# Optimization experiments

Measured on AMD Instinct MI355X. Metric: run time of the kernel, lower is better.

Reference implementation:

```python
import jax, jax.numpy as jnp
import numpy as np

B, NA, E, H = 256, 128, 1024, 16
HD = E // H  # head_dim = 64
EPS = 1e-5


def _ln(x, w, b):
    m = x.mean(-1, keepdims=True)
    v = x.var(-1, keepdims=True)
    return (x - m) / jnp.sqrt(v + EPS) * w + b


def setup_inputs() -> dict:
    key = jax.random.key(0)
    k0, k1 = jax.random.split(key)
    return {
        "x": jax.random.normal(k0, (B, NA, E), jnp.float32),
        "ln1_w": jnp.ones((E,), jnp.float32),
        "ln1_b": jnp.zeros((E,), jnp.float32),
        # xavier_uniform-ish scale for (3E, E)
        "in_w": jax.random.normal(k1, (3 * E, E), jnp.float32) * (1.0 / np.sqrt(E)),
        "in_b": jnp.zeros((3 * E,), jnp.float32),
        "ln2_w": jnp.ones((E,), jnp.float32),
        "ln2_b": jnp.zeros((E,), jnp.float32),
    }


def reference(x, ln1_w, ln1_b, in_w, in_b, ln2_w, ln2_b):
    bsz, na, e = x.shape
    xn = _ln(x, ln1_w, ln1_b)  # x = ln1(x) in the original (residual uses this)
    qkv = xn @ in_w.T + in_b  # (bsz, na, 3E)
    q, k, v = jnp.split(qkv, 3, axis=-1)
    q = q * (float(HD) ** -0.5)
    # Faithful to torch's contiguous().view(na, bsz*H, HD).transpose(0, 1):
    # a raw row-major reshape of the (bsz, na, E) buffer.
    def _heads(t):
        return t.reshape(na, bsz * H, HD).swapaxes(0, 1)  # (bsz*H, na, HD)
    q, k, v = _heads(q), _heads(k), _heads(v)
    scores = jnp.einsum('bnd,bmd->bnm', q, k)  # (bsz*H, na, na)
    w = jax.nn.softmax(scores, axis=-1)
    attn = jnp.einsum('bnm,bmd->bnd', w, v)  # (bsz*H, na, HD)
    attn = attn.swapaxes(0, 1).reshape(bsz, na, e)
    out = _ln(xn + attn, ln2_w, ln2_b)
    # Faithful quirk: sum over dim=1 (query dim) of (bsz*H, na, na), / num_heads
    avg_w = w.sum(axis=1) / H  # (bsz*H, na)
    return out, avg_w
```

## Files before the change

kernel.cpp:

```cpp
#include <hip/hip_runtime.h>


typedef __attribute__((ext_vector_type(4))) float float4v;
typedef __attribute__((ext_vector_type(4))) int   int4v;
typedef __attribute__((ext_vector_type(8))) short short8v;
typedef __attribute__((ext_vector_type(4))) short short4v;

#define LN_EPS 1e-5f

#define GLL(g, l) __builtin_amdgcn_global_load_lds( \
    (const __attribute__((address_space(1))) unsigned int*)(g), \
    (__attribute__((address_space(3))) unsigned int*)(l), 16, 0, 0)

__device__ __forceinline__ unsigned short f2bf(float f) {
    unsigned int u = __float_as_uint(f);
    u += 0x7FFFu + ((u >> 16) & 1u);
    return (unsigned short)(u >> 16);
}
__device__ __forceinline__ float bf2f(unsigned short h) {
    return __uint_as_float(((unsigned int)h) << 16);
}

__global__ __launch_bounds__(256) void k0_w_to_bf16(const float* __restrict__ w,
                                                    unsigned short* __restrict__ wb) {
    int idx = blockIdx.x * 256 + threadIdx.x;
    const float4v* src = (const float4v*)w;
    float4v a = src[idx * 2];
    float4v b = src[idx * 2 + 1];
    short8v o;
    o[0] = (short)f2bf(a[0]); o[1] = (short)f2bf(a[1]);
    o[2] = (short)f2bf(a[2]); o[3] = (short)f2bf(a[3]);
    o[4] = (short)f2bf(b[0]); o[5] = (short)f2bf(b[1]);
    o[6] = (short)f2bf(b[2]); o[7] = (short)f2bf(b[3]);
    *((short8v*)wb + idx) = o;
}

__global__ __launch_bounds__(256) void k1_ln1(const float* __restrict__ x,
                                              const float* __restrict__ w1,
                                              const float* __restrict__ b1,
                                              unsigned short* __restrict__ xnb) {
    int lane = threadIdx.x & 63;
    int wave = threadIdx.x >> 6;
    int row  = blockIdx.x * 4 + wave;
    const float4v* xr = (const float4v*)(x + (size_t)row * 1024);
    float4v xv[4];
    float s = 0.f, s2 = 0.f;
    #pragma unroll
    for (int c = 0; c < 4; ++c) {
        xv[c] = xr[c * 64 + lane];
        #pragma unroll
        for (int e = 0; e < 4; ++e) { s += xv[c][e]; s2 += xv[c][e] * xv[c][e]; }
    }
    #pragma unroll
    for (int off = 32; off > 0; off >>= 1) {
        s  += __shfl_xor(s, off, 64);
        s2 += __shfl_xor(s2, off, 64);
    }
    float mean = s * (1.0f / 1024.0f);
    float var  = s2 * (1.0f / 1024.0f) - mean * mean;
    float rs   = rsqrtf(var + LN_EPS);
    #pragma unroll
    for (int c = 0; c < 4; ++c) {
        int idx = c * 64 + lane;
        float4v wv = ((const float4v*)w1)[idx];
        float4v bv = ((const float4v*)b1)[idx];
        short4v o;
        #pragma unroll
        for (int e = 0; e < 4; ++e)
            o[e] = (short)f2bf((xv[c][e] - mean) * rs * wv[e] + bv[e]);
        ((short4v*)(xnb + (size_t)row * 1024))[idx] = o;
    }
}

__global__ __launch_bounds__(512, 2) void k2_qkv_gemm(const unsigned short* __restrict__ A,
                                                      const unsigned short* __restrict__ W,
                                                      const float* __restrict__ bias,
                                                      unsigned short* __restrict__ Qb,
                                                      unsigned short* __restrict__ Kb,
                                                      unsigned short* __restrict__ Vb) {
    __shared__ unsigned short smem[65536];
    unsigned short* sA0 = smem;
    unsigned short* sA1 = smem + 16384;
    unsigned short* sB0 = smem + 32768;
    unsigned short* sB1 = smem + 49152;

    int bid = blockIdx.x;
    int wg  = (bid & 7) * 192 + (bid >> 3);
    int nT  = wg % 12;
    int mT  = wg / 12;
    int rowBase = mT * 256;
    int colBase = nT * 256;

    int tid  = threadIdx.x;
    int lane = tid & 63;
    int wave = tid >> 6;
    int wm = wave >> 2, wn = wave & 3;
    int q4 = lane >> 4, l15 = lane & 15;

    int lrow_s = tid >> 3;
    int srcCol = ((tid & 7) * 16) ^ ((lrow_s & 7) << 4);
    const char* aSrc = (const char*)A + ((size_t)(rowBase + lrow_s) << 11) + srcCol;
    const char* wSrc = (const char*)W + ((size_t)(colBase + lrow_s) << 11) + srcCol;
    int waveOff = wave * 1024;

    int xorv = (l15 & 7) << 4;
    int aRow = (wm * 128 + l15) * 128;
    int bRow = (wn * 64 + l15) * 128;
    int bc0 = (q4 * 16) ^ xorv;
    int bc1 = (64 + q4 * 16) ^ xorv;

    float bv[4];
    #pragma unroll
    for (int n = 0; n < 4; ++n) bv[n] = bias[colBase + wn * 64 + n * 16 + l15];

    float4v acc[8][4];
    #pragma unroll
    for (int t = 0; t < 8; ++t)
        #pragma unroll
        for (int n = 0; n < 4; ++n) acc[t][n] = (float4v){0.f, 0.f, 0.f, 0.f};

#define STAGE_HALF(lds, src, ktB_, h) do { \
    GLL((src) + (ktB_) + (2*(h))   * 131072, (char*)(lds) + (2*(h))   * 8192 + waveOff); \
    GLL((src) + (ktB_) + (2*(h)+1) * 131072, (char*)(lds) + (2*(h)+1) * 8192 + waveOff); \
} while (0)
#define LDB(SB) do { \
    const char* c_ = (const char*)(SB); \
    _Pragma("unroll") \
    for (int n = 0; n < 4; ++n) { \
        bf[n][0] = *(const short8v*)(c_ + bRow + n * 2048 + bc0); \
        bf[n][1] = *(const short8v*)(c_ + bRow + n * 2048 + bc1); \
    } \
} while (0)
#define LDA2(SA, T0_) do { \
    const char* c_ = (const char*)(SA); \
    af[0][0] = *(const short8v*)(c_ + aRow + (T0_)     * 2048 + bc0); \
    af[0][1] = *(const short8v*)(c_ + aRow + (T0_)     * 2048 + bc1); \
    af[1][0] = *(const short8v*)(c_ + aRow + (T0_ + 1) * 2048 + bc0); \
    af[1][1] = *(const short8v*)(c_ + aRow + (T0_ + 1) * 2048 + bc1); \
} while (0)
#define MFMA8(T0_) do { \
    __builtin_amdgcn_s_setprio(1); \
    _Pragma("unroll") \
    for (int n = 0; n < 4; ++n) { \
        acc[T0_][n]     = __builtin_amdgcn_mfma_f32_16x16x32_bf16(af[0][0], bf[n][0], acc[T0_][n], 0, 0, 0); \
        acc[T0_][n]     = __builtin_amdgcn_mfma_f32_16x16x32_bf16(af[0][1], bf[n][1], acc[T0_][n], 0, 0, 0); \
        acc[T0_ + 1][n] = __builtin_amdgcn_mfma_f32_16x16x32_bf16(af[1][0], bf[n][0], acc[T0_ + 1][n], 0, 0, 0); \
        acc[T0_ + 1][n] = __builtin_amdgcn_mfma_f32_16x16x32_bf16(af[1][1], bf[n][1], acc[T0_ + 1][n], 0, 0, 0); \
    } \
    __builtin_amdgcn_s_setprio(0); \
} while (0)
#define PH_SYNC do { __builtin_amdgcn_s_barrier(); asm volatile("s_waitcnt lgkmcnt(0)"); } while (0)
#define PH_END  __builtin_amdgcn_s_barrier()

    STAGE_HALF(sA0, aSrc, 0, 0);
    STAGE_HALF(sA0, aSrc, 0, 1);
    STAGE_HALF(sB0, wSrc, 0, 0);
    STAGE_HALF(sB0, wSrc, 0, 1);
    STAGE_HALF(sB1, wSrc, 128, 0);
    STAGE_HALF(sB1, wSrc, 128, 1);
    asm volatile("s_waitcnt vmcnt(4)");
    __builtin_amdgcn_s_barrier();

    short8v af[2][2], bf[4][2];

    #pragma unroll 1
    for (int i = 0; i < 8; ++i) {
        int ktB = i << 8;
        bool nl = (i < 7);
        LDB(sB0); LDA2(sA0, 0);
        STAGE_HALF(sA1, aSrc, ktB + 128, 0);
        PH_SYNC; MFMA8(0); PH_END;
        LDA2(sA0, 2);
        STAGE_HALF(sA1, aSrc, ktB + 128, 1);
        PH_SYNC; MFMA8(2); PH_END;
        LDA2(sA0, 4);
        if (nl) STAGE_HALF(sB0, wSrc, ktB + 256, 0);
        PH_SYNC; MFMA8(4); PH_END;
        LDA2(sA0, 6);
        if (nl) { STAGE_HALF(sB0, wSrc, ktB + 256, 1); asm volatile("s_waitcnt vmcnt(4)"); }
        else    { asm volatile("s_waitcnt vmcnt(0)"); }
        PH_SYNC; MFMA8(6); PH_END;
        LDB(sB1); LDA2(sA1, 0);
        if (nl) STAGE_HALF(sA0, aSrc, ktB + 256, 0);
        PH_SYNC; MFMA8(0); PH_END;
        LDA2(sA1, 2);
        if (nl) STAGE_HALF(sA0, aSrc, ktB + 256, 1);
        PH_SYNC; MFMA8(2); PH_END;
        LDA2(sA1, 4);
        if (nl) STAGE_HALF(sB1, wSrc, ktB + 384, 0);
        PH_SYNC; MFMA8(4); PH_END;
        LDA2(sA1, 6);
        if (nl) { STAGE_HALF(sB1, wSrc, ktB + 384, 1); asm volatile("s_waitcnt vmcnt(4)"); }
        PH_SYNC; MFMA8(6); PH_END;
    }
#undef STAGE_HALF
#undef LDB
#undef LDA2
#undef MFMA8
#undef PH_SYNC
#undef PH_END

    __syncthreads();
    float scale = (colBase < 1024) ? 0.125f : 1.0f;
    unsigned short* outb = (colBase < 1024) ? Qb : (colBase < 2048) ? Kb : Vb;
    int lcol = colBase & 1023;
    #pragma unroll
    for (int t = 0; t < 8; ++t)
        #pragma unroll
        for (int n = 0; n < 4; ++n)
            #pragma unroll
            for (int g = 0; g < 4; ++g) {
                int row  = wm * 128 + t * 16 + q4 * 4 + g;
                int colb = (wn * 64 + n * 16 + l15) * 2;
                *(unsigned short*)((char*)smem + row * 512 + (colb ^ ((row & 7) << 4))) =
                    f2bf((acc[t][n][g] + bv[n]) * scale);
            }
    __syncthreads();
    #pragma unroll
    for (int k = 0; k < 16; ++k) {
        int r = k * 16 + (tid >> 5);
        short8v v = *(const short8v*)((const char*)smem + r * 512 + (tid & 31) * 16);
        int colb = ((tid & 31) * 16) ^ ((r & 7) << 4);
        *(short8v*)((char*)(outb + (size_t)(rowBase + r) * 1024 + lcol) + colb) = v;
    }
}

__global__ __launch_bounds__(256) void k2b_vtrans(const unsigned short* __restrict__ Vb,
                                                  unsigned short* __restrict__ Vt) {
    int g  = blockIdx.x * 256 + threadIdx.x;
    int ib = g & 15;
    int db = (g >> 4) & 7;
    int j  = g >> 7;
    const unsigned short* src = Vb + (size_t)(ib * 8) * 262144 + (size_t)j * 64 + db * 8;
    short8v in[8];
    #pragma unroll
    for (int r = 0; r < 8; ++r)
        in[r] = *(const short8v*)(src + (size_t)r * 262144);
    unsigned short* dst = Vt + (size_t)j * 8192 + (db * 8) * 128 + ib * 8;
    #pragma unroll
    for (int c = 0; c < 8; ++c) {
        short8v o;
        #pragma unroll
        for (int r = 0; r < 8; ++r) o[r] = in[r][c];
        *(short8v*)(dst + c * 128) = o;
    }
}

#define P_S  136
__global__ __launch_bounds__(256) void k3_attn(const unsigned short* __restrict__ Qb,
                                               const unsigned short* __restrict__ Kb,
                                               const unsigned short* __restrict__ Vt,
                                               unsigned short* __restrict__ attnb,
                                               float* __restrict__ avgw) {
    __shared__ unsigned short region0[17408];
    __shared__ float wred[2][2][128];
    __shared__ float colsum[128];
    unsigned short* sQ = region0;
    unsigned short* sK = region0 + 8192;
    unsigned short* sP = region0;

    int j = blockIdx.x;
    int tid = threadIdx.x;
    int lane = tid & 63;
    int wave = tid >> 6;
    int wm = wave >> 1, wn = wave & 1;
    int q4 = lane >> 4, l15 = lane & 15;
    size_t base = (size_t)j * 64;

    if (tid < 128) colsum[tid] = 0.f;

    {
        const char* qg = (const char*)(Qb + base);
        const char* kg = (const char*)(Kb + base);
        int swz = ((lane & 7) ^ (lane >> 3)) << 4;
        #pragma unroll
        for (int blk = 0; blk < 4; ++blk) {
            int row0 = wave * 32 + blk * 8;
            size_t src = (size_t)(row0 + (lane >> 3)) * 524288 + swz;
            GLL(qg + src, (char*)sQ + row0 * 128);
            GLL(kg + src, (char*)sK + row0 * 128);
        }
    }
    __syncthreads();

    const char* vg = (const char*)(Vt + (size_t)j * 8192);
    short8v vf[4][2];
    #pragma unroll
    for (int ks = 0; ks < 4; ++ks)
        #pragma unroll
        for (int t = 0; t < 2; ++t)
            vf[ks][t] = *(const short8v*)(vg + (wn * 32 + t * 16 + l15) * 256 + ks * 64 + q4 * 16);

    float4v zero4 = {0.f, 0.f, 0.f, 0.f};
    float4v S[4][4];
    #pragma unroll
    for (int a = 0; a < 4; ++a)
        #pragma unroll
        for (int b = 0; b < 4; ++b) S[a][b] = zero4;
    #pragma unroll
    for (int ks = 0; ks < 2; ++ks) {
        short8v qf[4], kf[4];
        #pragma unroll
        for (int t = 0; t < 4; ++t) {
            int rq = (wm * 64 + t * 16 + l15) * 128;
            int rk = (wn * 64 + t * 16 + l15) * 128;
            int cb = (ks * 64 + q4 * 16) ^ ((l15 & 7) << 4);
            qf[t] = *(const short8v*)((const char*)sQ + rq + cb);
            kf[t] = *(const short8v*)((const char*)sK + rk + cb);
        }
        #pragma unroll
        for (int tm = 0; tm < 4; ++tm)
            #pragma unroll
            for (int tn = 0; tn < 4; ++tn)
                S[tm][tn] = __builtin_amdgcn_mfma_f32_16x16x32_bf16(qf[tm], kf[tn], S[tm][tn], 0, 0, 0);
    }

    float rmax[4][4];
    #pragma unroll
    for (int tm = 0; tm < 4; ++tm)
        #pragma unroll
        for (int g = 0; g < 4; ++g)
            rmax[tm][g] = fmaxf(fmaxf(S[tm][0][g], S[tm][1][g]), fmaxf(S[tm][2][g], S[tm][3][g]));
    #pragma unroll
    for (int off = 1; off <= 8; off <<= 1)
        #pragma unroll
        for (int tm = 0; tm < 4; ++tm)
            #pragma unroll
            for (int g = 0; g < 4; ++g)
                rmax[tm][g] = fmaxf(rmax[tm][g], __shfl_xor(rmax[tm][g], off, 64));
    if (l15 == 0) {
        #pragma unroll
        for (int tm = 0; tm < 4; ++tm)
            #pragma unroll
            for (int g = 0; g < 4; ++g)
                wred[0][wn][wm * 64 + tm * 16 + q4 * 4 + g] = rmax[tm][g];
    }
    __syncthreads();

    float rsum[4][4];
    #pragma unroll
    for (int tm = 0; tm < 4; ++tm)
        #pragma unroll
        for (int g = 0; g < 4; ++g) {
            int r = wm * 64 + tm * 16 + q4 * 4 + g;
            float rm = fmaxf(wred[0][0][r], wred[0][1][r]);
            float t0 = 0.f;
            #pragma unroll
            for (int tn = 0; tn < 4; ++tn) {
                float e = __expf(S[tm][tn][g] - rm);
                S[tm][tn][g] = e;
                t0 += e;
            }
            rsum[tm][g] = t0;
        }
    #pragma unroll
    for (int off = 1; off <= 8; off <<= 1)
        #pragma unroll
        for (int tm = 0; tm < 4; ++tm)
            #pragma unroll
            for (int g = 0; g < 4; ++g)
                rsum[tm][g] += __shfl_xor(rsum[tm][g], off, 64);
    if (l15 == 0) {
        #pragma unroll
        for (int tm = 0; tm < 4; ++tm)
            #pragma unroll
            for (int g = 0; g < 4; ++g)
                wred[1][wn][wm * 64 + tm * 16 + q4 * 4 + g] = rsum[tm][g];
    }
    __syncthreads();

    #pragma unroll
    for (int tm = 0; tm < 4; ++tm)
        #pragma unroll
        for (int g = 0; g < 4; ++g) {
            int r = wm * 64 + tm * 16 + q4 * 4 + g;
            float inv = 1.0f / (wred[1][0][r] + wred[1][1][r]);
            #pragma unroll
            for (int tn = 0; tn < 4; ++tn) S[tm][tn][g] *= inv;
        }

    float cs[4];
    #pragma unroll
    for (int tn = 0; tn < 4; ++tn) {
        float t0 = 0.f;
        #pragma unroll
        for (int tm = 0; tm < 4; ++tm)
            #pragma unroll
            for (int g = 0; g < 4; ++g) t0 += S[tm][tn][g];
        cs[tn] = t0;
    }
    #pragma unroll
    for (int off = 16; off <= 32; off <<= 1)
        #pragma unroll
        for (int tn = 0; tn < 4; ++tn) cs[tn] += __shfl_xor(cs[tn], off, 64);
    if (lane < 16) {
        #pragma unroll
        for (int tn = 0; tn < 4; ++tn)
            atomicAdd(&colsum[wn * 64 + tn * 16 + lane], cs[tn]);
    }
    __syncthreads();

    #pragma unroll
    for (int tm = 0; tm < 4; ++tm)
        #pragma unroll
        for (int tn = 0; tn < 4; ++tn)
            #pragma unroll
            for (int g = 0; g < 4; ++g)
                sP[(wm * 64 + tm * 16 + q4 * 4 + g) * P_S + wn * 64 + tn * 16 + l15] = f2bf(S[tm][tn][g]);
    __syncthreads();

    if (tid < 128) avgw[(size_t)j * 128 + tid] = colsum[tid] * (1.0f / 16.0f);

    float4v O[4][2];
    #pragma unroll
    for (int a = 0; a < 4; ++a) { O[a][0] = zero4; O[a][1] = zero4; }
    #pragma unroll
    for (int ks = 0; ks < 4; ++ks) {
        short8v pf[4];
        #pragma unroll
        for (int t = 0; t < 4; ++t)
            pf[t] = *(const short8v*)(sP + (wm * 64 + t * 16 + l15) * P_S + q4 * 8 + ks * 32);
        #pragma unroll
        for (int tm = 0; tm < 4; ++tm)
            #pragma unroll
            for (int tn = 0; tn < 2; ++tn)
                O[tm][tn] = __builtin_amdgcn_mfma_f32_16x16x32_bf16(pf[tm], vf[ks][tn], O[tm][tn], 0, 0, 0);
    }
    #pragma unroll
    for (int tm = 0; tm < 4; ++tm)
        #pragma unroll
        for (int tn = 0; tn < 2; ++tn)
            #pragma unroll
            for (int g = 0; g < 4; ++g) {
                int i = wm * 64 + tm * 16 + q4 * 4 + g;
                int d = wn * 32 + tn * 16 + l15;
                attnb[base + (size_t)i * 262144 + d] = f2bf(O[tm][tn][g]);
            }
}

__global__ __launch_bounds__(256) void k4_ln2(const float* __restrict__ x,
                                              const float* __restrict__ w1,
                                              const float* __restrict__ b1,
                                              const unsigned short* __restrict__ attnb,
                                              const float* __restrict__ w2,
                                              const float* __restrict__ b2,
                                              float* __restrict__ out) {
    int lane = threadIdx.x & 63;
    int wave = threadIdx.x >> 6;
    int row  = blockIdx.x * 4 + wave;
    const float4v* xr = (const float4v*)(x + (size_t)row * 1024);
    float4v xv[4];
    float s = 0.f, s2 = 0.f;
    #pragma unroll
    for (int c = 0; c < 4; ++c) {
        xv[c] = xr[c * 64 + lane];
        #pragma unroll
        for (int e = 0; e < 4; ++e) { s += xv[c][e]; s2 += xv[c][e] * xv[c][e]; }
    }
    #pragma unroll
    for (int off = 32; off > 0; off >>= 1) {
        s  += __shfl_xor(s, off, 64);
        s2 += __shfl_xor(s2, off, 64);
    }
    float mean = s * (1.0f / 1024.0f);
    float var  = s2 * (1.0f / 1024.0f) - mean * mean;
    float rs   = rsqrtf(var + LN_EPS);
    float4v r[4];
    s = 0.f; s2 = 0.f;
    #pragma unroll
    for (int c = 0; c < 4; ++c) {
        int idx = c * 64 + lane;
        float4v wv = ((const float4v*)w1)[idx];
        float4v bv = ((const float4v*)b1)[idx];
        short4v av = ((const short4v*)(attnb + (size_t)row * 1024))[idx];
        #pragma unroll
        for (int e = 0; e < 4; ++e) {
            r[c][e] = (xv[c][e] - mean) * rs * wv[e] + bv[e] + bf2f((unsigned short)av[e]);
            s += r[c][e]; s2 += r[c][e] * r[c][e];
        }
    }
    #pragma unroll
    for (int off = 32; off > 0; off >>= 1) {
        s  += __shfl_xor(s, off, 64);
        s2 += __shfl_xor(s2, off, 64);
    }
    float mean2 = s * (1.0f / 1024.0f);
    float var2  = s2 * (1.0f / 1024.0f) - mean2 * mean2;
    float rs2   = rsqrtf(var2 + LN_EPS);
    #pragma unroll
    for (int c = 0; c < 4; ++c) {
        int idx = c * 64 + lane;
        float4v w2v = ((const float4v*)w2)[idx];
        float4v b2v = ((const float4v*)b2)[idx];
        float4v o;
        #pragma unroll
        for (int e = 0; e < 4; ++e)
            o[e] = (r[c][e] - mean2) * rs2 * w2v[e] + b2v[e];
        ((float4v*)(out + (size_t)row * 1024))[idx] = o;
    }
}

extern "C" void kernel_launch(void* const* d_in, const int* in_sizes, int n_in,
                              void* d_out, int out_size, void* d_ws, size_t ws_size,
                              hipStream_t stream) {
    const float* x    = (const float*)d_in[0];
    const float* ln1w = (const float*)d_in[1];
    const float* ln1b = (const float*)d_in[2];
    const float* inw  = (const float*)d_in[3];
    const float* inb  = (const float*)d_in[4];
    const float* ln2w = (const float*)d_in[5];
    const float* ln2b = (const float*)d_in[6];
    float* out  = (float*)d_out;
    float* avgw = out + 33554432;

    char* ws = (char*)d_ws;
    unsigned short* xnb   = (unsigned short*)(ws);
    unsigned short* Vt    = (unsigned short*)(ws);
    unsigned short* Qb    = (unsigned short*)(ws + 67108864);
    unsigned short* Kb    = (unsigned short*)(ws + 134217728);
    unsigned short* Vb    = (unsigned short*)(ws + 201326592);
    unsigned short* attnb = (unsigned short*)(ws + 201326592);
    unsigned short* Wb    = (unsigned short*)(ws + 268435456);

    k0_w_to_bf16<<<1536, 256, 0, stream>>>(inw, Wb);
    k1_ln1<<<8192, 256, 0, stream>>>(x, ln1w, ln1b, xnb);
    k2_qkv_gemm<<<1536, 512, 0, stream>>>(xnb, Wb, inb, Qb, Kb, Vb);
    k2b_vtrans<<<2048, 256, 0, stream>>>(Vb, Vt);
    k3_attn<<<4096, 256, 0, stream>>>(Qb, Kb, Vt, attnb, avgw);
    k4_ln2<<<8192, 256, 0, stream>>>(x, ln1w, ln1b, attnb, ln2w, ln2b, out);
}
```

Before: 613.0 us.

## Restructure attention kernel: two heads per block, wave owns full score rows

The attention kernel now processes two heads per block, and each pair of waves splits one head by query rows, so every wave holds complete 128-wide score rows. It computes S transposed (K×Q) so that the row max and sum need only cross-lane shuffles, which removes the cross-wave LDS reductions and most of the block barriers. Each wave gets a private P buffer in LDS, writes bf16 values packed in pairs with v_cvt_pk_bf16, and double-buffers its V fragment loads across the PV k-steps. In exchange it uses more LDS per block (about 68KB), which may lower occupancy, and the score accumulators double per wave, which raises register pressure.

```diff
diff --git a/kernel.cpp b/kernel.cpp
--- a/kernel.cpp
+++ b/kernel.cpp
@@ -19,6 +19,11 @@
 }
 __device__ __forceinline__ float bf2f(unsigned short h) {
     return __uint_as_float(((unsigned int)h) << 16);
+}
+__device__ __forceinline__ unsigned int pk_bf16(float lo, float hi) {
+    unsigned int r;
+    asm("v_cvt_pk_bf16_f32 %0, %1, %2" : "=v"(r) : "v"(lo), "v"(hi));
+    return r;
 }
 
 __global__ __launch_bounds__(256) void k0_w_to_bf16(const float* __restrict__ w,
@@ -246,36 +251,35 @@
     }
 }
 
-#define P_S  136
 __global__ __launch_bounds__(256) void k3_attn(const unsigned short* __restrict__ Qb,
                                                const unsigned short* __restrict__ Kb,
                                                const unsigned short* __restrict__ Vt,
                                                unsigned short* __restrict__ attnb,
                                                float* __restrict__ avgw) {
-    __shared__ unsigned short region0[17408];
-    __shared__ float wred[2][2][128];
-    __shared__ float colsum[128];
-    unsigned short* sQ = region0;
-    unsigned short* sK = region0 + 8192;
-    unsigned short* sP = region0;
-
-    int j = blockIdx.x;
+    __shared__ unsigned short smem[34816];
+    __shared__ float csum[2][2][128];
+
     int tid = threadIdx.x;
     int lane = tid & 63;
     int wave = tid >> 6;
-    int wm = wave >> 1, wn = wave & 1;
+    int grp = wave >> 1, wm = wave & 1;
+    int j = blockIdx.x * 2 + grp;
     int q4 = lane >> 4, l15 = lane & 15;
-    size_t base = (size_t)j * 64;
-
-    if (tid < 128) colsum[tid] = 0.f;
+
+    unsigned short* sQ = smem + grp * 8192;
+    unsigned short* sK = smem + 16384 + grp * 8192;
+    char* sP = (char*)smem + wave * 17408;
+
+    csum[0][tid >> 7][tid & 127] = 0.f;
+    csum[1][tid >> 7][tid & 127] = 0.f;
 
     {
-        const char* qg = (const char*)(Qb + base);
-        const char* kg = (const char*)(Kb + base);
+        const char* qg = (const char*)(Qb + (size_t)j * 64);
+        const char* kg = (const char*)(Kb + (size_t)j * 64);
         int swz = ((lane & 7) ^ (lane >> 3)) << 4;
         #pragma unroll
-        for (int blk = 0; blk < 4; ++blk) {
-            int row0 = wave * 32 + blk * 8;
+        for (int blk = 0; blk < 8; ++blk) {
+            int row0 = wm * 64 + blk * 8;
             size_t src = (size_t)(row0 + (lane >> 3)) * 524288 + swz;
             GLL(qg + src, (char*)sQ + row0 * 128);
             GLL(kg + src, (char*)sK + row0 * 128);
@@ -283,159 +287,135 @@
     }
     __syncthreads();
 
-    const char* vg = (const char*)(Vt + (size_t)j * 8192);
-    short8v vf[4][2];
-    #pragma unroll
-    for (int ks = 0; ks < 4; ++ks)
-        #pragma unroll
-        for (int t = 0; t < 2; ++t)
-            vf[ks][t] = *(const short8v*)(vg + (wn * 32 + t * 16 + l15) * 256 + ks * 64 + q4 * 16);
-
-    float4v zero4 = {0.f, 0.f, 0.f, 0.f};
-    float4v S[4][4];
-    #pragma unroll
-    for (int a = 0; a < 4; ++a)
-        #pragma unroll
-        for (int b = 0; b < 4; ++b) S[a][b] = zero4;
+    float4v S[8][4];
+    #pragma unroll
+    for (int a = 0; a < 8; ++a)
+        #pragma unroll
+        for (int b = 0; b < 4; ++b) S[a][b] = (float4v){0.f, 0.f, 0.f, 0.f};
     #pragma unroll
     for (int ks = 0; ks < 2; ++ks) {
-        short8v qf[4], kf[4];
-        #pragma unroll
-        for (int t = 0; t < 4; ++t) {
-            int rq = (wm * 64 + t * 16 + l15) * 128;
-            int rk = (wn * 64 + t * 16 + l15) * 128;
-            int cb = (ks * 64 + q4 * 16) ^ ((l15 & 7) << 4);
-            qf[t] = *(const short8v*)((const char*)sQ + rq + cb);
-            kf[t] = *(const short8v*)((const char*)sK + rk + cb);
+        int cb = (ks * 64 + q4 * 16) ^ ((l15 & 7) << 4);
+        short8v qf[4];
+        #pragma unroll
+        for (int tm = 0; tm < 4; ++tm)
+            qf[tm] = *(const short8v*)((const char*)sQ + (wm * 64 + tm * 16 + l15) * 128 + cb);
+        #pragma unroll
+        for (int tn = 0; tn < 8; ++tn) {
+            short8v kf = *(const short8v*)((const char*)sK + (tn * 16 + l15) * 128 + cb);
+            #pragma unroll
+            for (int tm = 0; tm < 4; ++tm)
+                S[tn][tm] = __builtin_amdgcn_mfma_f32_16x16x32_bf16(kf, qf[tm], S[tn][tm], 0, 0, 0);
         }
-        #pragma unroll
-        for (int tm = 0; tm < 4; ++tm)
-            #pragma unroll
-            for (int tn = 0; tn < 4; ++tn)
-                S[tm][tn] = __builtin_amdgcn_mfma_f32_16x16x32_bf16(qf[tm], kf[tn], S[tm][tn], 0, 0, 0);
-    }
-
-    float rmax[4][4];
-    #pragma unroll
-    for (int tm = 0; tm < 4; ++tm)
-        #pragma unroll
-        for (int g = 0; g < 4; ++g)
-            rmax[tm][g] = fmaxf(fmaxf(S[tm][0][g], S[tm][1][g]), fmaxf(S[tm][2][g], S[tm][3][g]));
-    #pragma unroll
-    for (int off = 1; off <= 8; off <<= 1)
-        #pragma unroll
-        for (int tm = 0; tm < 4; ++tm)
-            #pragma unroll
-            for (int g = 0; g < 4; ++g)
-                rmax[tm][g] = fmaxf(rmax[tm][g], __shfl_xor(rmax[tm][g], off, 64));
-    if (l15 == 0) {
-        #pragma unroll
-        for (int tm = 0; tm < 4; ++tm)
-            #pragma unroll
-            for (int g = 0; g < 4; ++g)
-                wred[0][wn][wm * 64 + tm * 16 + q4 * 4 + g] = rmax[tm][g];
     }
     __syncthreads();
 
-    float rsum[4][4];
-    #pragma unroll
-    for (int tm = 0; tm < 4; ++tm)
-        #pragma unroll
-        for (int g = 0; g < 4; ++g) {
-            int r = wm * 64 + tm * 16 + q4 * 4 + g;
-            float rm = fmaxf(wred[0][0][r], wred[0][1][r]);
-            float t0 = 0.f;
-            #pragma unroll
-            for (int tn = 0; tn < 4; ++tn) {
-                float e = __expf(S[tm][tn][g] - rm);
-                S[tm][tn][g] = e;
+    const char* vg = (const char*)Vt + (size_t)j * 16384;
+    short8v vf0[4], vf1[4];
+    #pragma unroll
+    for (int t = 0; t < 4; ++t)
+        vf0[t] = *(const short8v*)(vg + (t * 16 + l15) * 256 + q4 * 16);
+
+    float rmax[4], inv[4];
+    #pragma unroll
+    for (int tm = 0; tm < 4; ++tm) {
+        float m0 = S[0][tm][0];
+        #pragma unroll
+        for (int tn = 0; tn < 8; ++tn)
+            #pragma unroll
+            for (int g = 0; g < 4; ++g) m0 = fmaxf(m0, S[tn][tm][g]);
+        m0 = fmaxf(m0, __shfl_xor(m0, 16, 64));
+        m0 = fmaxf(m0, __shfl_xor(m0, 32, 64));
+        rmax[tm] = m0;
+    }
+    #pragma unroll
+    for (int tm = 0; tm < 4; ++tm) {
+        float t0 = 0.f;
+        #pragma unroll
+        for (int tn = 0; tn < 8; ++tn)
+            #pragma unroll
+            for (int g = 0; g < 4; ++g) {
+                float e = __expf(S[tn][tm][g] - rmax[tm]);
+                S[tn][tm][g] = e;
                 t0 += e;
             }
-            rsum[tm][g] = t0;
+        t0 += __shfl_xor(t0, 16, 64);
+        t0 += __shfl_xor(t0, 32, 64);
+        inv[tm] = 1.0f / t0;
+    }
+    #pragma unroll
+    for (int tn = 0; tn < 8; ++tn)
+        #pragma unroll
+        for (int tm = 0; tm < 4; ++tm)
+            #pragma unroll
+            for (int g = 0; g < 4; ++g) S[tn][tm][g] *= inv[tm];
+
+    #pragma unroll
+    for (int tn = 0; tn < 8; ++tn) {
+        #pragma unroll
+        for (int g = 0; g < 4; ++g) {
+            float cs = S[tn][0][g] + S[tn][1][g] + S[tn][2][g] + S[tn][3][g];
+            cs += __shfl_xor(cs, 1, 64);
+            cs += __shfl_xor(cs, 2, 64);
+            cs += __shfl_xor(cs, 4, 64);
+            cs += __shfl_xor(cs, 8, 64);
+            if (l15 == 0) csum[wm][grp][tn * 16 + q4 * 4 + g] = cs;
         }
-    #pragma unroll
-    for (int off = 1; off <= 8; off <<= 1)
+    }
+
+    #pragma unroll
+    for (int tn = 0; tn < 8; ++tn)
         #pragma unroll
         for (int tm = 0; tm < 4; ++tm)
             #pragma unroll
-            for (int g = 0; g < 4; ++g)
-                rsum[tm][g] += __shfl_xor(rsum[tm][g], off, 64);
-    if (l15 == 0) {
+            for (int p = 0; p < 2; ++p) {
+                unsigned int pk = pk_bf16(S[tn][tm][2 * p], S[tn][tm][2 * p + 1]);
+                *(unsigned int*)(sP + (tm * 16 + l15) * 272 +
+                                 (tn * 16 + q4 * 4 + 2 * p) * 2) = pk;
+            }
+
+    float4v O[4][4];
+    #pragma unroll
+    for (int a = 0; a < 4; ++a)
+        #pragma unroll
+        for (int b = 0; b < 4; ++b) O[a][b] = (float4v){0.f, 0.f, 0.f, 0.f};
+    #pragma unroll
+    for (int ks = 0; ks < 4; ++ks) {
+        if (ks < 3) {
+            #pragma unroll
+            for (int t = 0; t < 4; ++t)
+                vf1[t] = *(const short8v*)(vg + (t * 16 + l15) * 256 + (ks + 1) * 64 + q4 * 16);
+        }
+        short8v pf[4];
         #pragma unroll
         for (int tm = 0; tm < 4; ++tm)
-            #pragma unroll
-            for (int g = 0; g < 4; ++g)
-                wred[1][wn][wm * 64 + tm * 16 + q4 * 4 + g] = rsum[tm][g];
-    }
+            pf[tm] = *(const short8v*)(sP + (tm * 16 + l15) * 272 + ks * 64 + q4 * 16);
+        #pragma unroll
+        for (int tm = 0; tm < 4; ++tm)
+            #pragma unroll
+            for (int tno = 0; tno < 4; ++tno)
+                O[tm][tno] = __builtin_amdgcn_mfma_f32_16x16x32_bf16(pf[tm], vf0[tno], O[tm][tno], 0, 0, 0);
+        #pragma unroll
+        for (int t = 0; t < 4; ++t) vf0[t] = vf1[t];
+    }
+
+    size_t base = (size_t)j * 64;
+    #pragma unroll
+    for (int tm = 0; tm < 4; ++tm)
+        #pragma unroll
+        for (int tno = 0; tno < 4; ++tno)
+            #pragma unroll
+            for (int g = 0; g < 4; ++g) {
+                int m = wm * 64 + tm * 16 + q4 * 4 + g;
+                int d = tno * 16 + l15;
+                attnb[base + (size_t)m * 262144 + d] = f2bf(O[tm][tno][g]);
+            }
+
     __syncthreads();
-
-    #pragma unroll
-    for (int tm = 0; tm < 4; ++tm)
-        #pragma unroll
-        for (int g = 0; g < 4; ++g) {
-            int r = wm * 64 + tm * 16 + q4 * 4 + g;
-            float inv = 1.0f / (wred[1][0][r] + wred[1][1][r]);
-            #pragma unroll
-            for (int tn = 0; tn < 4; ++tn) S[tm][tn][g] *= inv;
-        }
-
-    float cs[4];
-    #pragma unroll
-    for (int tn = 0; tn < 4; ++tn) {
-        float t0 = 0.f;
-        #pragma unroll
-        for (int tm = 0; tm < 4; ++tm)
-            #pragma unroll
-            for (int g = 0; g < 4; ++g) t0 += S[tm][tn][g];
-        cs[tn] = t0;
-    }
-    #pragma unroll
-    for (int off = 16; off <= 32; off <<= 1)
-        #pragma unroll
-        for (int tn = 0; tn < 4; ++tn) cs[tn] += __shfl_xor(cs[tn], off, 64);
-    if (lane < 16) {
-        #pragma unroll
-        for (int tn = 0; tn < 4; ++tn)
-            atomicAdd(&colsum[wn * 64 + tn * 16 + lane], cs[tn]);
-    }
-    __syncthreads();
-
-    #pragma unroll
-    for (int tm = 0; tm < 4; ++tm)
-        #pragma unroll
-        for (int tn = 0; tn < 4; ++tn)
-            #pragma unroll
-            for (int g = 0; g < 4; ++g)
-                sP[(wm * 64 + tm * 16 + q4 * 4 + g) * P_S + wn * 64 + tn * 16 + l15] = f2bf(S[tm][tn][g]);
-    __syncthreads();
-
-    if (tid < 128) avgw[(size_t)j * 128 + tid] = colsum[tid] * (1.0f / 16.0f);
-
-    float4v O[4][2];
-    #pragma unroll
-    for (int a = 0; a < 4; ++a) { O[a][0] = zero4; O[a][1] = zero4; }
-    #pragma unroll
-    for (int ks = 0; ks < 4; ++ks) {
-        short8v pf[4];
-        #pragma unroll
-        for (int t = 0; t < 4; ++t)
-            pf[t] = *(const short8v*)(sP + (wm * 64 + t * 16 + l15) * P_S + q4 * 8 + ks * 32);
-        #pragma unroll
-        for (int tm = 0; tm < 4; ++tm)
-            #pragma unroll
-            for (int tn = 0; tn < 2; ++tn)
-                O[tm][tn] = __builtin_amdgcn_mfma_f32_16x16x32_bf16(pf[tm], vf[ks][tn], O[tm][tn], 0, 0, 0);
-    }
-    #pragma unroll
-    for (int tm = 0; tm < 4; ++tm)
-        #pragma unroll
-        for (int tn = 0; tn < 2; ++tn)
-            #pragma unroll
-            for (int g = 0; g < 4; ++g) {
-                int i = wm * 64 + tm * 16 + q4 * 4 + g;
-                int d = wn * 32 + tn * 16 + l15;
-                attnb[base + (size_t)i * 262144 + d] = f2bf(O[tm][tn][g]);
-            }
+    {
+        int g2 = tid >> 7, n = tid & 127;
+        avgw[(size_t)(blockIdx.x * 2 + g2) * 128 + n] =
+            (csum[0][g2][n] + csum[1][g2][n]) * (1.0f / 16.0f);
+    }
 }
 
 __global__ __launch_bounds__(256) void k4_ln2(const float* __restrict__ x,
@@ -526,6 +506,6 @@
     k1_ln1<<<8192, 256, 0, stream>>>(x, ln1w, ln1b, xnb);
     k2_qkv_gemm<<<1536, 512, 0, stream>>>(xnb, Wb, inb, Qb, Kb, Vb);
     k2b_vtrans<<<2048, 256, 0, stream>>>(Vb, Vt);
-    k3_attn<<<4096, 256, 0, stream>>>(Qb, Kb, Vt, attnb, avgw);
+    k3_attn<<<2048, 256, 0, stream>>>(Qb, Kb, Vt, attnb, avgw);
     k4_ln2<<<8192, 256, 0, stream>>>(x, ln1w, ln1b, attnb, ln2w, ln2b, out);
 }
```

Result: slower. 632.3 us (+3.1%).
